# Optimization experiments

Hardware: AMD Instinct MI355X
Metric: run time of the kernel (lower is better)

## Reference

```python
import jax, jax.numpy as jnp
import numpy as np

BATCH = 1048576
D_IN = 4        # d_in=3 spatial dims + 1 time dim
HID = 64
N_HID_STACK = 4  # hidden residual blocks after the first hidden layer
D_OUT = 3
BN_EPS = 1e-5


def _bn(x, gamma, beta):
    # BatchNorm1d in training mode: biased batch statistics over the batch axis
    mu = jnp.mean(x, axis=0)
    var = jnp.var(x, axis=0)
    return gamma * (x - mu) * jax.lax.rsqrt(var + BN_EPS) + beta


def setup_inputs() -> dict:
    key = jax.random.key(0)
    ks = jax.random.split(key, 8)
    s_in = 1.0 / np.sqrt(D_IN)
    s_h = 1.0 / np.sqrt(HID)
    return {
        "x": jax.random.normal(ks[0], (BATCH, D_IN), dtype=jnp.float32),
        "bn0_gamma": jnp.ones((D_IN,), jnp.float32),
        "bn0_beta": jnp.zeros((D_IN,), jnp.float32),
        "W0": jax.random.normal(ks[1], (D_IN, HID), jnp.float32) * s_in,
        "b0": jnp.zeros((HID,), jnp.float32),
        "gamma0": jnp.ones((HID,), jnp.float32),
        "beta0": jnp.zeros((HID,), jnp.float32),
        "W_hid": jax.random.normal(ks[2], (N_HID_STACK, HID, HID), jnp.float32) * s_h,
        "b_hid": jnp.zeros((N_HID_STACK, HID), jnp.float32),
        "gamma_hid": jnp.ones((N_HID_STACK, HID), jnp.float32),
        "beta_hid": jnp.zeros((N_HID_STACK, HID), jnp.float32),
        "Wout": jax.random.normal(ks[3], (HID, D_OUT), jnp.float32) * s_h,
        "bout": jnp.zeros((D_OUT,), jnp.float32),
    }


def reference(x, bn0_gamma, bn0_beta, W0, b0, gamma0, beta0,
              W_hid, b_hid, gamma_hid, beta_hid, Wout, bout):
    # Net.forward (u-network, single patch, batch_normalization=True, tanh):
    #   x = bn0(x)
    #   y = bn(act(Linear0(x)))                 (first hidden layer, no skip)
    #   y = bn_i(act(Linear_i(y))) + y          (residual hidden layers)
    #   y = Linear_out(y)
    h = _bn(x, bn0_gamma, bn0_beta)
    y = _bn(jnp.tanh(h @ W0 + b0), gamma0, beta0)

    def step(y, layer):
        W, b, g, be = layer
        return _bn(jnp.tanh(y @ W + b), g, be) + y, None

    y, _ = jax.lax.scan(step, y, (W_hid, b_hid, gamma_hid, beta_hid))
    return y @ Wout + bout
```

## Files before the change

### kernel.cpp

```cpp
#include <hip/hip_runtime.h>
#include <stdint.h>


#define NROWS 1048576
#define EPS 1e-5f
#define INV_B 9.5367431640625e-07f
#define LOG2E2 2.885390081777927f
#define BIGGRID 16384

typedef __attribute__((ext_vector_type(8))) short bfrag;
typedef __attribute__((ext_vector_type(4))) float facc;
typedef __attribute__((ext_vector_type(4))) float f4v;

__device__ __forceinline__ float bf2f(short s) {
  union { unsigned u; float f; } v;
  v.u = ((unsigned)(unsigned short)s) << 16;
  return v.f;
}
__device__ __forceinline__ short f2bf(float f) {
  union { float f; unsigned u; } v;
  v.f = f;
  unsigned r = v.u + 0x7FFFu + ((v.u >> 16) & 1u);
  return (short)(r >> 16);
}
__device__ __forceinline__ float tanh_fast(float x) {
  float e = __builtin_amdgcn_exp2f(x * LOG2E2);
  return 1.f - 2.f * __builtin_amdgcn_rcpf(e + 1.f);
}

template <int W>
__global__ __launch_bounds__(256) void k_reduce(const float* __restrict__ P,
                                                float* __restrict__ S,
                                                int rows_per_blk) {
  __shared__ float red[256];
  const int tid = threadIdx.x;
  const int col = tid % W;
  const int grp = tid / W;
  const int G = 256 / W;
  size_t r0 = (size_t)blockIdx.x * rows_per_blk;
  float s = 0.f;
  for (int r = grp; r < rows_per_blk; r += G) s += P[(r0 + r) * W + col];
  red[tid] = s;
  __syncthreads();
  if (tid < W) {
    float t = 0.f;
#pragma unroll 4
    for (int g = 0; g < G; ++g) t += red[g * W + tid];
    atomicAdd(&S[tid], t);
  }
}


__global__ __launch_bounds__(256) void k_stats_x(const float* __restrict__ x,
                                                 float* __restrict__ P) {
  __shared__ float red[4][8];
  const int tid = threadIdx.x;
  const int wave = tid >> 6;
  size_t base = (size_t)blockIdx.x * 1024 + tid;
  float s[4] = {0.f, 0.f, 0.f, 0.f}, q[4] = {0.f, 0.f, 0.f, 0.f};
#pragma unroll
  for (int it = 0; it < 4; ++it) {
    f4v v = *(const f4v*)(x + (base + (size_t)it * 256) * 4);
#pragma unroll
    for (int k = 0; k < 4; ++k) { s[k] += v[k]; q[k] = fmaf(v[k], v[k], q[k]); }
  }
#pragma unroll
  for (int off = 32; off > 0; off >>= 1) {
#pragma unroll
    for (int k = 0; k < 4; ++k) {
      s[k] += __shfl_xor(s[k], off);
      q[k] += __shfl_xor(q[k], off);
    }
  }
  if ((tid & 63) == 0) {
#pragma unroll
    for (int k = 0; k < 4; ++k) { red[wave][k] = s[k]; red[wave][4 + k] = q[k]; }
  }
  __syncthreads();
  if (tid < 8)
    P[blockIdx.x * 8 + tid] =
        red[0][tid] + red[1][tid] + red[2][tid] + red[3][tid];
}

__global__ __launch_bounds__(256) void k_stats_z1(
    const float* __restrict__ x, const float* __restrict__ bn0g,
    const float* __restrict__ bn0b, const float* __restrict__ W0,
    const float* __restrict__ b0, const float* __restrict__ sx,
    float* __restrict__ P) {
  __shared__ float red[2][4][64];
  const int tid = threadIdx.x;
  const int lane = tid & 63;
  const int wave = tid >> 6;
  int gw = blockIdx.x * 4 + wave;
  float sc[4], sh[4];
#pragma unroll
  for (int k = 0; k < 4; ++k) {
    float mean = sx[k] * INV_B;
    float var = fmaf(-mean, mean, sx[4 + k] * INV_B);
    float rs = rsqrtf(var + EPS);
    sc[k] = bn0g[k] * rs;
    sh[k] = fmaf(-sc[k], mean, bn0b[k]);
  }
  float w[4];
#pragma unroll
  for (int k = 0; k < 4; ++k) w[k] = W0[k * 64 + lane];
  float bj = b0[lane];
  float s = 0.f, q = 0.f;
  size_t r0 = (size_t)gw * 256;
  for (int r = 0; r < 256; ++r) {
    f4v xv = *(const f4v*)(x + (r0 + r) * 4);
    float acc = bj;
#pragma unroll
    for (int k = 0; k < 4; ++k)
      acc = fmaf(fmaf(xv[k], sc[k], sh[k]), w[k], acc);
    float z = tanh_fast(acc);
    s += z;
    q = fmaf(z, z, q);
  }
  red[0][wave][lane] = s;
  red[1][wave][lane] = q;
  __syncthreads();
  if (tid < 128) {
    int which = tid >> 6, c = tid & 63;
    P[blockIdx.x * 128 + tid] = red[which][0][c] + red[which][1][c] +
                                red[which][2][c] + red[which][3][c];
  }
}

__global__ __launch_bounds__(256) void k_prep(const float* __restrict__ Wh,
                                              short* __restrict__ WT) {
  int idx = blockIdx.x * 256 + threadIdx.x;
  int l = idx >> 12, rem = idx & 4095, k = rem >> 6, c = rem & 63;
  WT[l * 4096 + c * 64 + k] = f2bf(Wh[l * 4096 + k * 64 + c]);
}


__global__ __launch_bounds__(128) void k_first(
    const float* __restrict__ x, const float* __restrict__ bn0g,
    const float* __restrict__ bn0b, const float* __restrict__ W0,
    const float* __restrict__ b0, const float* __restrict__ gamma0,
    const float* __restrict__ beta0, const float* __restrict__ sx,
    const float* __restrict__ s1, const short* __restrict__ WTb,
    const float* __restrict__ bb, float* __restrict__ P,
    short* __restrict__ Y) {
  __shared__ __align__(16) float lds_x[64 * 4];
  __shared__ __align__(16) short lds_y[64 * 72];
  __shared__ float lds_st[128];

  const int tid = threadIdx.x;
  const int lane = tid & 63;
  const int wave = tid >> 6;
  const int l15 = lane & 15;
  const int q = lane >> 4;
  const int wr = wave * 32;
  const size_t r0 = (size_t)blockIdx.x * 64;

  f4v xp;
  if (lane < 32) xp = *(const f4v*)(x + (r0 + wr + lane) * 4);

  lds_st[tid] = 0.f;
  float sc0[4], sh0[4];
#pragma unroll
  for (int k = 0; k < 4; ++k) {
    float mean = sx[k] * INV_B;
    float var = fmaf(-mean, mean, sx[4 + k] * INV_B);
    float rs = rsqrtf(var + EPS);
    sc0[k] = bn0g[k] * rs;
    sh0[k] = fmaf(-sc0[k], mean, bn0b[k]);
  }
  float w0c[4];
#pragma unroll
  for (int k = 0; k < 4; ++k) w0c[k] = W0[k * 64 + lane];
  float b0c = b0[lane];
  float mean1 = s1[lane] * INV_B;
  float var1 = fmaf(-mean1, mean1, s1[64 + lane] * INV_B);
  float A1c = gamma0[lane] * rsqrtf(var1 + EPS);
  float B1c = fmaf(-A1c, mean1, beta0[lane]);
  if (lane < 32) *(f4v*)&lds_x[(wr + lane) * 4] = xp;
  __syncthreads();

  for (int e = 0; e < 32; ++e) {
    int row = wr + e;
    float acc = b0c;
#pragma unroll
    for (int k = 0; k < 4; ++k)
      acc = fmaf(fmaf(lds_x[row * 4 + k], sc0[k], sh0[k]), w0c[k], acc);
    float z = tanh_fast(acc);
    lds_y[row * 72 + lane] = f2bf(fmaf(A1c, z, B1c));
  }

  bfrag af[2][2];
#pragma unroll
  for (int mt = 0; mt < 2; ++mt)
#pragma unroll
    for (int kt = 0; kt < 2; ++kt) {
      af[mt][kt] =
          *(const bfrag*)&lds_y[(wr + mt * 16 + l15) * 72 + kt * 32 + q * 8];
      *(bfrag*)(Y + (r0 + wr + mt * 16 + l15) * 64 + kt * 32 + q * 8) =
          af[mt][kt];
    }
  float bbv[4];
  bfrag bwb[4][2];
#pragma unroll
  for (int nt = 0; nt < 4; ++nt) {
    bbv[nt] = bb[nt * 16 + l15];
#pragma unroll
    for (int kt = 0; kt < 2; ++kt)
      bwb[nt][kt] =
          *(const bfrag*)(WTb + (nt * 16 + l15) * 64 + kt * 32 + q * 8);
  }
  facc acc2[2][4];
#pragma unroll
  for (int mt = 0; mt < 2; ++mt)
#pragma unroll
    for (int nt = 0; nt < 4; ++nt) {
      acc2[mt][nt][0] = bbv[nt]; acc2[mt][nt][1] = bbv[nt];
      acc2[mt][nt][2] = bbv[nt]; acc2[mt][nt][3] = bbv[nt];
    }
#pragma unroll
  for (int mt = 0; mt < 2; ++mt)
#pragma unroll
    for (int nt = 0; nt < 4; ++nt)
#pragma unroll
      for (int kt = 0; kt < 2; ++kt)
        acc2[mt][nt] = __builtin_amdgcn_mfma_f32_16x16x32_bf16(
            af[mt][kt], bwb[nt][kt], acc2[mt][nt], 0, 0, 0);
  float sAcc[4], qAcc[4];
#pragma unroll
  for (int nt = 0; nt < 4; ++nt) {
    sAcc[nt] = 0.f;
    qAcc[nt] = 0.f;
#pragma unroll
    for (int mt = 0; mt < 2; ++mt)
#pragma unroll
      for (int i = 0; i < 4; ++i) {
        float z = tanh_fast(acc2[mt][nt][i]);
        sAcc[nt] += z;
        qAcc[nt] = fmaf(z, z, qAcc[nt]);
      }
    float s = sAcc[nt], ss = qAcc[nt];
    s += __shfl_xor(s, 16); s += __shfl_xor(s, 32);
    ss += __shfl_xor(ss, 16); ss += __shfl_xor(ss, 32);
    if (q == 0) {
      atomicAdd(&lds_st[nt * 16 + l15], s);
      atomicAdd(&lds_st[64 + nt * 16 + l15], ss);
    }
  }
  __syncthreads();
  P[(size_t)blockIdx.x * 128 + tid] = lds_st[tid];
}

__global__ __launch_bounds__(128) void k_mid(
    short* __restrict__ Y, const short* __restrict__ WTa,
    const float* __restrict__ ba, const float* __restrict__ ga,
    const float* __restrict__ bea, const float* __restrict__ sa,
    const short* __restrict__ WTb, const float* __restrict__ bb,
    float* __restrict__ P) {
  __shared__ __align__(16) short lds_y[64 * 72];
  __shared__ float lds_st[128];

  const int tid = threadIdx.x;
  const int lane = tid & 63;
  const int wave = tid >> 6;
  const int l15 = lane & 15;
  const int q = lane >> 4;
  const int wr = wave * 32;
  const size_t r0 = (size_t)blockIdx.x * 64;
  const int srow = lane >> 3;
  const int sc8 = (lane & 7) * 8;

  bfrag ld[4];
  {
    const size_t g = (r0 + wr + srow) * 64 + sc8;
#pragma unroll
    for (int it = 0; it < 4; ++it)
      ld[it] = *(const bfrag*)(Y + g + (size_t)it * 8 * 64);
  }

  lds_st[tid] = 0.f;
  float Av[4], Bv[4], bav[4];
#pragma unroll
  for (int nt = 0; nt < 4; ++nt) {
    int c = nt * 16 + l15;
    float mean = sa[c] * INV_B;
    float var = fmaf(-mean, mean, sa[64 + c] * INV_B);
    float A = ga[c] * rsqrtf(var + EPS);
    Av[nt] = A;
    Bv[nt] = fmaf(-A, mean, bea[c]);
    bav[nt] = ba[c];
  }
  bfrag bwa[4][2];
#pragma unroll
  for (int nt = 0; nt < 4; ++nt)
#pragma unroll
    for (int kt = 0; kt < 2; ++kt)
      bwa[nt][kt] =
          *(const bfrag*)(WTa + (nt * 16 + l15) * 64 + kt * 32 + q * 8);

#pragma unroll
  for (int it = 0; it < 4; ++it)
    *(bfrag*)&lds_y[(wr + it * 8 + srow) * 72 + sc8] = ld[it];
  __syncthreads();

  bfrag af[2][2];
#pragma unroll
  for (int mt = 0; mt < 2; ++mt)
#pragma unroll
    for (int kt = 0; kt < 2; ++kt)
      af[mt][kt] =
          *(const bfrag*)&lds_y[(wr + mt * 16 + l15) * 72 + kt * 32 + q * 8];
  facc acc[2][4];
#pragma unroll
  for (int mt = 0; mt < 2; ++mt)
#pragma unroll
    for (int nt = 0; nt < 4; ++nt) {
      acc[mt][nt][0] = bav[nt]; acc[mt][nt][1] = bav[nt];
      acc[mt][nt][2] = bav[nt]; acc[mt][nt][3] = bav[nt];
    }
#pragma unroll
  for (int mt = 0; mt < 2; ++mt)
#pragma unroll
    for (int nt = 0; nt < 4; ++nt)
#pragma unroll
      for (int kt = 0; kt < 2; ++kt)
        acc[mt][nt] = __builtin_amdgcn_mfma_f32_16x16x32_bf16(
            af[mt][kt], bwa[nt][kt], acc[mt][nt], 0, 0, 0);

#pragma unroll
  for (int mt = 0; mt < 2; ++mt)
#pragma unroll
    for (int nt = 0; nt < 4; ++nt) {
      int c = nt * 16 + l15;
      float A = Av[nt], Bc = Bv[nt];
#pragma unroll
      for (int i = 0; i < 4; ++i) {
        int rl = wr + mt * 16 + q * 4 + i;
        float z = tanh_fast(acc[mt][nt][i]);
        float yo = bf2f(lds_y[rl * 72 + c]);
        lds_y[rl * 72 + c] = f2bf(fmaf(A, z, Bc) + yo);
      }
    }

#pragma unroll
  for (int mt = 0; mt < 2; ++mt)
#pragma unroll
    for (int kt = 0; kt < 2; ++kt) {
      af[mt][kt] =
          *(const bfrag*)&lds_y[(wr + mt * 16 + l15) * 72 + kt * 32 + q * 8];
      *(bfrag*)(Y + (r0 + wr + mt * 16 + l15) * 64 + kt * 32 + q * 8) =
          af[mt][kt];
    }
  float bbv[4];
  bfrag bwb[4][2];
#pragma unroll
  for (int nt = 0; nt < 4; ++nt) {
    bbv[nt] = bb[nt * 16 + l15];
#pragma unroll
    for (int kt = 0; kt < 2; ++kt)
      bwb[nt][kt] =
          *(const bfrag*)(WTb + (nt * 16 + l15) * 64 + kt * 32 + q * 8);
  }
#pragma unroll
  for (int mt = 0; mt < 2; ++mt)
#pragma unroll
    for (int nt = 0; nt < 4; ++nt) {
      acc[mt][nt][0] = bbv[nt]; acc[mt][nt][1] = bbv[nt];
      acc[mt][nt][2] = bbv[nt]; acc[mt][nt][3] = bbv[nt];
    }
#pragma unroll
  for (int mt = 0; mt < 2; ++mt)
#pragma unroll
    for (int nt = 0; nt < 4; ++nt)
#pragma unroll
      for (int kt = 0; kt < 2; ++kt)
        acc[mt][nt] = __builtin_amdgcn_mfma_f32_16x16x32_bf16(
            af[mt][kt], bwb[nt][kt], acc[mt][nt], 0, 0, 0);
#pragma unroll
  for (int nt = 0; nt < 4; ++nt) {
    float s = 0.f, ss = 0.f;
#pragma unroll
    for (int mt = 0; mt < 2; ++mt)
#pragma unroll
      for (int i = 0; i < 4; ++i) {
        float z = tanh_fast(acc[mt][nt][i]);
        s += z;
        ss = fmaf(z, z, ss);
      }
    s += __shfl_xor(s, 16); s += __shfl_xor(s, 32);
    ss += __shfl_xor(ss, 16); ss += __shfl_xor(ss, 32);
    if (q == 0) {
      atomicAdd(&lds_st[nt * 16 + l15], s);
      atomicAdd(&lds_st[64 + nt * 16 + l15], ss);
    }
  }
  __syncthreads();
  P[(size_t)blockIdx.x * 128 + tid] = lds_st[tid];
}

__global__ __launch_bounds__(128) void k_last(
    const short* __restrict__ Y, const short* __restrict__ WTa,
    const float* __restrict__ ba, const float* __restrict__ ga,
    const float* __restrict__ bea, const float* __restrict__ sa,
    const float* __restrict__ Wout, const float* __restrict__ bout,
    float* __restrict__ out) {
  __shared__ __align__(16) short lds_y[64 * 72];
  __shared__ float lds_wo[192];

  const int tid = threadIdx.x;
  const int lane = tid & 63;
  const int wave = tid >> 6;
  const int l15 = lane & 15;
  const int q = lane >> 4;
  const int wr = wave * 32;
  const size_t r0 = (size_t)blockIdx.x * 64;
  const int srow = lane >> 3;
  const int sc8 = (lane & 7) * 8;

  bfrag ld[4];
  {
    const size_t g = (r0 + wr + srow) * 64 + sc8;
#pragma unroll
    for (int it = 0; it < 4; ++it)
      ld[it] = *(const bfrag*)(Y + g + (size_t)it * 8 * 64);
  }

  for (int i = tid; i < 192; i += 128) lds_wo[i] = Wout[i];
  float Av[4], Bv[4], bav[4];
#pragma unroll
  for (int nt = 0; nt < 4; ++nt) {
    int c = nt * 16 + l15;
    float mean = sa[c] * INV_B;
    float var = fmaf(-mean, mean, sa[64 + c] * INV_B);
    float A = ga[c] * rsqrtf(var + EPS);
    Av[nt] = A;
    Bv[nt] = fmaf(-A, mean, bea[c]);
    bav[nt] = ba[c];
  }
  bfrag bwa[4][2];
#pragma unroll
  for (int nt = 0; nt < 4; ++nt)
#pragma unroll
    for (int kt = 0; kt < 2; ++kt)
      bwa[nt][kt] =
          *(const bfrag*)(WTa + (nt * 16 + l15) * 64 + kt * 32 + q * 8);
  float bo0 = bout[0], bo1 = bout[1], bo2 = bout[2];

#pragma unroll
  for (int it = 0; it < 4; ++it)
    *(bfrag*)&lds_y[(wr + it * 8 + srow) * 72 + sc8] = ld[it];
  __syncthreads();

  bfrag af[2][2];
#pragma unroll
  for (int mt = 0; mt < 2; ++mt)
#pragma unroll
    for (int kt = 0; kt < 2; ++kt)
      af[mt][kt] =
          *(const bfrag*)&lds_y[(wr + mt * 16 + l15) * 72 + kt * 32 + q * 8];
  facc acc[2][4];
#pragma unroll
  for (int mt = 0; mt < 2; ++mt)
#pragma unroll
    for (int nt = 0; nt < 4; ++nt) {
      acc[mt][nt][0] = bav[nt]; acc[mt][nt][1] = bav[nt];
      acc[mt][nt][2] = bav[nt]; acc[mt][nt][3] = bav[nt];
    }
#pragma unroll
  for (int mt = 0; mt < 2; ++mt)
#pragma unroll
    for (int nt = 0; nt < 4; ++nt)
#pragma unroll
      for (int kt = 0; kt < 2; ++kt)
        acc[mt][nt] = __builtin_amdgcn_mfma_f32_16x16x32_bf16(
            af[mt][kt], bwa[nt][kt], acc[mt][nt], 0, 0, 0);
#pragma unroll
  for (int mt = 0; mt < 2; ++mt)
#pragma unroll
    for (int nt = 0; nt < 4; ++nt) {
      int c = nt * 16 + l15;
      float A = Av[nt], Bc = Bv[nt];
#pragma unroll
      for (int i = 0; i < 4; ++i) {
        int rl = wr + mt * 16 + q * 4 + i;
        float z = tanh_fast(acc[mt][nt][i]);
        float yo = bf2f(lds_y[rl * 72 + c]);
        lds_y[rl * 72 + c] = f2bf(fmaf(A, z, Bc) + yo);
      }
    }

  {
    int row = wr + (lane >> 1);
    int cb = (lane & 1) * 32;
    float o0 = 0.f, o1 = 0.f, o2 = 0.f;
#pragma unroll
    for (int jc = 0; jc < 4; ++jc) {
      bfrag v = *(const bfrag*)&lds_y[row * 72 + cb + jc * 8];
#pragma unroll
      for (int j = 0; j < 8; ++j) {
        float f = bf2f(v[j]);
        int jj = cb + jc * 8 + j;
        o0 = fmaf(f, lds_wo[jj * 3 + 0], o0);
        o1 = fmaf(f, lds_wo[jj * 3 + 1], o1);
        o2 = fmaf(f, lds_wo[jj * 3 + 2], o2);
      }
    }
    o0 += __shfl_xor(o0, 1);
    o1 += __shfl_xor(o1, 1);
    o2 += __shfl_xor(o2, 1);
    if ((lane & 1) == 0) {
      size_t ro = (r0 + row) * 3;
      out[ro] = o0 + bo0;
      out[ro + 1] = o1 + bo1;
      out[ro + 2] = o2 + bo2;
    }
  }
}

extern "C" void kernel_launch(void* const* d_in, const int* in_sizes, int n_in,
                              void* d_out, int out_size, void* d_ws,
                              size_t ws_size, hipStream_t stream) {
  (void)in_sizes; (void)n_in; (void)out_size; (void)ws_size;
  const float* x = (const float*)d_in[0];
  const float* bn0g = (const float*)d_in[1];
  const float* bn0b = (const float*)d_in[2];
  const float* W0 = (const float*)d_in[3];
  const float* b0 = (const float*)d_in[4];
  const float* gamma0 = (const float*)d_in[5];
  const float* beta0 = (const float*)d_in[6];
  const float* Wh = (const float*)d_in[7];
  const float* bh = (const float*)d_in[8];
  const float* gh = (const float*)d_in[9];
  const float* beh = (const float*)d_in[10];
  const float* Wout = (const float*)d_in[11];
  const float* bout = (const float*)d_in[12];
  float* out = (float*)d_out;

  char* ws = (char*)d_ws;
  short* Y = (short*)ws;
  const size_t YB = (size_t)NROWS * 64 * 2;
  float* stats = (float*)(ws + YB);
  float* Sx = stats;
  float* S1 = stats + 8;
  float* S2 = stats + 136;
  float* S3 = stats + 264;
  float* S4 = stats + 392;
  float* S5 = stats + 520;
  short* WT = (short*)(ws + YB + 4096);
  float* P = (float*)(ws + YB + 4096 + 32768);

  hipMemsetAsync(stats, 0, 648 * sizeof(float), stream);
  k_prep<<<64, 256, 0, stream>>>(Wh, WT);
  k_stats_x<<<1024, 256, 0, stream>>>(x, P);
  k_reduce<8><<<8, 256, 0, stream>>>(P, Sx, 128);
  k_stats_z1<<<1024, 256, 0, stream>>>(x, bn0g, bn0b, W0, b0, Sx, P);
  k_reduce<128><<<8, 256, 0, stream>>>(P, S1, 128);
  k_first<<<BIGGRID, 128, 0, stream>>>(x, bn0g, bn0b, W0, b0, gamma0, beta0,
                                       Sx, S1, WT, bh, P, Y);
  k_reduce<128><<<128, 256, 0, stream>>>(P, S2, 128);
  k_mid<<<BIGGRID, 128, 0, stream>>>(Y, WT, bh, gh, beh, S2, WT + 4096,
                                     bh + 64, P);
  k_reduce<128><<<128, 256, 0, stream>>>(P, S3, 128);
  k_mid<<<BIGGRID, 128, 0, stream>>>(Y, WT + 4096, bh + 64, gh + 64, beh + 64,
                                     S3, WT + 2 * 4096, bh + 128, P);
  k_reduce<128><<<128, 256, 0, stream>>>(P, S4, 128);
  k_mid<<<BIGGRID, 128, 0, stream>>>(Y, WT + 2 * 4096, bh + 128, gh + 128,
                                     beh + 128, S4, WT + 3 * 4096, bh + 192, P);
  k_reduce<128><<<128, 256, 0, stream>>>(P, S5, 128);
  k_last<<<BIGGRID, 128, 0, stream>>>(Y, WT + 3 * 4096, bh + 192, gh + 192,
                                      beh + 192, S5, Wout, bout, out);
}
```

Before: 562.4 us.

## Use single-wave blocks processing two 32-row tiles with register prefetch

The main per-layer kernels now run with one 64-thread wave per block instead of two. Each wave handles both 32-row halves of its 64-row tile in sequence, prefetching the second half's activations into registers while the first half computes. This removes __syncthreads and the LDS atomics for the stats partials, which are now written directly from registers. It also loads Y fragments directly in MFMA layout rather than staging them through LDS. The cost is less in-block parallelism and a serial dependency between the two halves, while LDS per block is smaller, which may allow more blocks resident per CU.

```diff
diff --git a/kernel.cpp b/kernel.cpp
--- a/kernel.cpp
+++ b/kernel.cpp
@@ -135,7 +135,7 @@
 }
 
 
-__global__ __launch_bounds__(128) void k_first(
+__global__ __launch_bounds__(64) void k_first(
     const float* __restrict__ x, const float* __restrict__ bn0g,
     const float* __restrict__ bn0b, const float* __restrict__ W0,
     const float* __restrict__ b0, const float* __restrict__ gamma0,
@@ -143,22 +143,17 @@
     const float* __restrict__ s1, const short* __restrict__ WTb,
     const float* __restrict__ bb, float* __restrict__ P,
     short* __restrict__ Y) {
-  __shared__ __align__(16) float lds_x[64 * 4];
-  __shared__ __align__(16) short lds_y[64 * 72];
-  __shared__ float lds_st[128];
-
-  const int tid = threadIdx.x;
-  const int lane = tid & 63;
-  const int wave = tid >> 6;
+  __shared__ __align__(16) float lds_x[32 * 4];
+  __shared__ __align__(16) short ly[32 * 72];
+
+  const int lane = threadIdx.x & 63;
   const int l15 = lane & 15;
   const int q = lane >> 4;
-  const int wr = wave * 32;
   const size_t r0 = (size_t)blockIdx.x * 64;
 
   f4v xp;
-  if (lane < 32) xp = *(const f4v*)(x + (r0 + wr + lane) * 4);
-
-  lds_st[tid] = 0.f;
+  if (lane < 32) xp = *(const f4v*)(x + (r0 + lane) * 4);
+
   float sc0[4], sh0[4];
 #pragma unroll
   for (int k = 0; k < 4; ++k) {
@@ -176,29 +171,6 @@
   float var1 = fmaf(-mean1, mean1, s1[64 + lane] * INV_B);
   float A1c = gamma0[lane] * rsqrtf(var1 + EPS);
   float B1c = fmaf(-A1c, mean1, beta0[lane]);
-  if (lane < 32) *(f4v*)&lds_x[(wr + lane) * 4] = xp;
-  __syncthreads();
-
-  for (int e = 0; e < 32; ++e) {
-    int row = wr + e;
-    float acc = b0c;
-#pragma unroll
-    for (int k = 0; k < 4; ++k)
-      acc = fmaf(fmaf(lds_x[row * 4 + k], sc0[k], sh0[k]), w0c[k], acc);
-    float z = tanh_fast(acc);
-    lds_y[row * 72 + lane] = f2bf(fmaf(A1c, z, B1c));
-  }
-
-  bfrag af[2][2];
-#pragma unroll
-  for (int mt = 0; mt < 2; ++mt)
-#pragma unroll
-    for (int kt = 0; kt < 2; ++kt) {
-      af[mt][kt] =
-          *(const bfrag*)&lds_y[(wr + mt * 16 + l15) * 72 + kt * 32 + q * 8];
-      *(bfrag*)(Y + (r0 + wr + mt * 16 + l15) * 64 + kt * 32 + q * 8) =
-          af[mt][kt];
-    }
   float bbv[4];
   bfrag bwb[4][2];
 #pragma unroll
@@ -209,75 +181,95 @@
       bwb[nt][kt] =
           *(const bfrag*)(WTb + (nt * 16 + l15) * 64 + kt * 32 + q * 8);
   }
-  facc acc2[2][4];
-#pragma unroll
-  for (int mt = 0; mt < 2; ++mt)
-#pragma unroll
-    for (int nt = 0; nt < 4; ++nt) {
-      acc2[mt][nt][0] = bbv[nt]; acc2[mt][nt][1] = bbv[nt];
-      acc2[mt][nt][2] = bbv[nt]; acc2[mt][nt][3] = bbv[nt];
-    }
-#pragma unroll
-  for (int mt = 0; mt < 2; ++mt)
+
+  float sAcc[4] = {0.f, 0.f, 0.f, 0.f}, qAcc[4] = {0.f, 0.f, 0.f, 0.f};
+
+#pragma unroll
+  for (int t = 0; t < 2; ++t) {
+    const size_t rt = r0 + t * 32;
+    if (lane < 32) *(f4v*)&lds_x[lane * 4] = xp;
+    if (t == 0 && lane < 32) xp = *(const f4v*)(x + (r0 + 32 + lane) * 4);
+
+    for (int e = 0; e < 32; ++e) {
+      float acc = b0c;
+#pragma unroll
+      for (int k = 0; k < 4; ++k)
+        acc = fmaf(fmaf(lds_x[e * 4 + k], sc0[k], sh0[k]), w0c[k], acc);
+      float z = tanh_fast(acc);
+      ly[e * 72 + lane] = f2bf(fmaf(A1c, z, B1c));
+    }
+
+    bfrag af[2][2];
+#pragma unroll
+    for (int mt = 0; mt < 2; ++mt)
+#pragma unroll
+      for (int kt = 0; kt < 2; ++kt) {
+        af[mt][kt] =
+            *(const bfrag*)&ly[(mt * 16 + l15) * 72 + kt * 32 + q * 8];
+        *(bfrag*)(Y + (rt + mt * 16 + l15) * 64 + kt * 32 + q * 8) =
+            af[mt][kt];
+      }
+    facc acc2[2][4];
+#pragma unroll
+    for (int mt = 0; mt < 2; ++mt)
+#pragma unroll
+      for (int nt = 0; nt < 4; ++nt) {
+        acc2[mt][nt][0] = bbv[nt]; acc2[mt][nt][1] = bbv[nt];
+        acc2[mt][nt][2] = bbv[nt]; acc2[mt][nt][3] = bbv[nt];
+      }
+#pragma unroll
+    for (int mt = 0; mt < 2; ++mt)
+#pragma unroll
+      for (int nt = 0; nt < 4; ++nt)
+#pragma unroll
+        for (int kt = 0; kt < 2; ++kt)
+          acc2[mt][nt] = __builtin_amdgcn_mfma_f32_16x16x32_bf16(
+              af[mt][kt], bwb[nt][kt], acc2[mt][nt], 0, 0, 0);
 #pragma unroll
     for (int nt = 0; nt < 4; ++nt)
 #pragma unroll
-      for (int kt = 0; kt < 2; ++kt)
-        acc2[mt][nt] = __builtin_amdgcn_mfma_f32_16x16x32_bf16(
-            af[mt][kt], bwb[nt][kt], acc2[mt][nt], 0, 0, 0);
-  float sAcc[4], qAcc[4];
+      for (int mt = 0; mt < 2; ++mt)
+#pragma unroll
+        for (int i = 0; i < 4; ++i) {
+          float z = tanh_fast(acc2[mt][nt][i]);
+          sAcc[nt] += z;
+          qAcc[nt] = fmaf(z, z, qAcc[nt]);
+        }
+  }
+
 #pragma unroll
   for (int nt = 0; nt < 4; ++nt) {
-    sAcc[nt] = 0.f;
-    qAcc[nt] = 0.f;
-#pragma unroll
-    for (int mt = 0; mt < 2; ++mt)
-#pragma unroll
-      for (int i = 0; i < 4; ++i) {
-        float z = tanh_fast(acc2[mt][nt][i]);
-        sAcc[nt] += z;
-        qAcc[nt] = fmaf(z, z, qAcc[nt]);
-      }
     float s = sAcc[nt], ss = qAcc[nt];
     s += __shfl_xor(s, 16); s += __shfl_xor(s, 32);
     ss += __shfl_xor(ss, 16); ss += __shfl_xor(ss, 32);
     if (q == 0) {
-      atomicAdd(&lds_st[nt * 16 + l15], s);
-      atomicAdd(&lds_st[64 + nt * 16 + l15], ss);
-    }
-  }
-  __syncthreads();
-  P[(size_t)blockIdx.x * 128 + tid] = lds_st[tid];
-}
-
-__global__ __launch_bounds__(128) void k_mid(
+      P[(size_t)blockIdx.x * 128 + nt * 16 + l15] = s;
+      P[(size_t)blockIdx.x * 128 + 64 + nt * 16 + l15] = ss;
+    }
+  }
+}
+
+__global__ __launch_bounds__(64) void k_mid(
     short* __restrict__ Y, const short* __restrict__ WTa,
     const float* __restrict__ ba, const float* __restrict__ ga,
     const float* __restrict__ bea, const float* __restrict__ sa,
     const short* __restrict__ WTb, const float* __restrict__ bb,
     float* __restrict__ P) {
-  __shared__ __align__(16) short lds_y[64 * 72];
-  __shared__ float lds_st[128];
-
-  const int tid = threadIdx.x;
-  const int lane = tid & 63;
-  const int wave = tid >> 6;
+  __shared__ __align__(16) short ly[32 * 72];
+
+  const int lane = threadIdx.x & 63;
   const int l15 = lane & 15;
   const int q = lane >> 4;
-  const int wr = wave * 32;
   const size_t r0 = (size_t)blockIdx.x * 64;
-  const int srow = lane >> 3;
-  const int sc8 = (lane & 7) * 8;
-
-  bfrag ld[4];
-  {
-    const size_t g = (r0 + wr + srow) * 64 + sc8;
-#pragma unroll
-    for (int it = 0; it < 4; ++it)
-      ld[it] = *(const bfrag*)(Y + g + (size_t)it * 8 * 64);
-  }
-
-  lds_st[tid] = 0.f;
+
+  bfrag afn[2][2];
+#pragma unroll
+  for (int mt = 0; mt < 2; ++mt)
+#pragma unroll
+    for (int kt = 0; kt < 2; ++kt)
+      afn[mt][kt] =
+          *(const bfrag*)(Y + (r0 + mt * 16 + l15) * 64 + kt * 32 + q * 8);
+
   float Av[4], Bv[4], bav[4];
 #pragma unroll
   for (int nt = 0; nt < 4; ++nt) {
@@ -297,134 +289,142 @@
       bwa[nt][kt] =
           *(const bfrag*)(WTa + (nt * 16 + l15) * 64 + kt * 32 + q * 8);
 
-#pragma unroll
-  for (int it = 0; it < 4; ++it)
-    *(bfrag*)&lds_y[(wr + it * 8 + srow) * 72 + sc8] = ld[it];
-  __syncthreads();
-
-  bfrag af[2][2];
-#pragma unroll
-  for (int mt = 0; mt < 2; ++mt)
-#pragma unroll
-    for (int kt = 0; kt < 2; ++kt)
-      af[mt][kt] =
-          *(const bfrag*)&lds_y[(wr + mt * 16 + l15) * 72 + kt * 32 + q * 8];
-  facc acc[2][4];
-#pragma unroll
-  for (int mt = 0; mt < 2; ++mt)
+  float sAcc[4] = {0.f, 0.f, 0.f, 0.f}, qAcc[4] = {0.f, 0.f, 0.f, 0.f};
+
+#pragma unroll
+  for (int t = 0; t < 2; ++t) {
+    const size_t rt = r0 + t * 32;
+    bfrag af[2][2];
+#pragma unroll
+    for (int mt = 0; mt < 2; ++mt)
+#pragma unroll
+      for (int kt = 0; kt < 2; ++kt) {
+        af[mt][kt] = afn[mt][kt];
+        *(bfrag*)&ly[(mt * 16 + l15) * 72 + kt * 32 + q * 8] = af[mt][kt];
+      }
+    if (t == 0) {
+#pragma unroll
+      for (int mt = 0; mt < 2; ++mt)
+#pragma unroll
+        for (int kt = 0; kt < 2; ++kt)
+          afn[mt][kt] = *(const bfrag*)(Y + (r0 + 32 + mt * 16 + l15) * 64 +
+                                        kt * 32 + q * 8);
+    }
+
+    facc acc[2][4];
+#pragma unroll
+    for (int mt = 0; mt < 2; ++mt)
+#pragma unroll
+      for (int nt = 0; nt < 4; ++nt) {
+        acc[mt][nt][0] = bav[nt]; acc[mt][nt][1] = bav[nt];
+        acc[mt][nt][2] = bav[nt]; acc[mt][nt][3] = bav[nt];
+      }
+#pragma unroll
+    for (int mt = 0; mt < 2; ++mt)
+#pragma unroll
+      for (int nt = 0; nt < 4; ++nt)
+#pragma unroll
+        for (int kt = 0; kt < 2; ++kt)
+          acc[mt][nt] = __builtin_amdgcn_mfma_f32_16x16x32_bf16(
+              af[mt][kt], bwa[nt][kt], acc[mt][nt], 0, 0, 0);
+
+#pragma unroll
+    for (int mt = 0; mt < 2; ++mt)
+#pragma unroll
+      for (int nt = 0; nt < 4; ++nt) {
+        int c = nt * 16 + l15;
+        float A = Av[nt], Bc = Bv[nt];
+#pragma unroll
+        for (int i = 0; i < 4; ++i) {
+          int rl = mt * 16 + q * 4 + i;
+          float z = tanh_fast(acc[mt][nt][i]);
+          float yo = bf2f(ly[rl * 72 + c]);
+          ly[rl * 72 + c] = f2bf(fmaf(A, z, Bc) + yo);
+        }
+      }
+
+    bfrag af2[2][2];
+#pragma unroll
+    for (int mt = 0; mt < 2; ++mt)
+#pragma unroll
+      for (int kt = 0; kt < 2; ++kt) {
+        af2[mt][kt] =
+            *(const bfrag*)&ly[(mt * 16 + l15) * 72 + kt * 32 + q * 8];
+        *(bfrag*)(Y + (rt + mt * 16 + l15) * 64 + kt * 32 + q * 8) =
+            af2[mt][kt];
+      }
+    float bbv[4];
+    bfrag bwb[4][2];
 #pragma unroll
     for (int nt = 0; nt < 4; ++nt) {
-      acc[mt][nt][0] = bav[nt]; acc[mt][nt][1] = bav[nt];
-      acc[mt][nt][2] = bav[nt]; acc[mt][nt][3] = bav[nt];
-    }
-#pragma unroll
-  for (int mt = 0; mt < 2; ++mt)
+      bbv[nt] = bb[nt * 16 + l15];
+#pragma unroll
+      for (int kt = 0; kt < 2; ++kt)
+        bwb[nt][kt] =
+            *(const bfrag*)(WTb + (nt * 16 + l15) * 64 + kt * 32 + q * 8);
+    }
+#pragma unroll
+    for (int mt = 0; mt < 2; ++mt)
+#pragma unroll
+      for (int nt = 0; nt < 4; ++nt) {
+        acc[mt][nt][0] = bbv[nt]; acc[mt][nt][1] = bbv[nt];
+        acc[mt][nt][2] = bbv[nt]; acc[mt][nt][3] = bbv[nt];
+      }
+#pragma unroll
+    for (int mt = 0; mt < 2; ++mt)
+#pragma unroll
+      for (int nt = 0; nt < 4; ++nt)
+#pragma unroll
+        for (int kt = 0; kt < 2; ++kt)
+          acc[mt][nt] = __builtin_amdgcn_mfma_f32_16x16x32_bf16(
+              af2[mt][kt], bwb[nt][kt], acc[mt][nt], 0, 0, 0);
 #pragma unroll
     for (int nt = 0; nt < 4; ++nt)
 #pragma unroll
-      for (int kt = 0; kt < 2; ++kt)
-        acc[mt][nt] = __builtin_amdgcn_mfma_f32_16x16x32_bf16(
-            af[mt][kt], bwa[nt][kt], acc[mt][nt], 0, 0, 0);
-
-#pragma unroll
-  for (int mt = 0; mt < 2; ++mt)
-#pragma unroll
-    for (int nt = 0; nt < 4; ++nt) {
-      int c = nt * 16 + l15;
-      float A = Av[nt], Bc = Bv[nt];
-#pragma unroll
-      for (int i = 0; i < 4; ++i) {
-        int rl = wr + mt * 16 + q * 4 + i;
-        float z = tanh_fast(acc[mt][nt][i]);
-        float yo = bf2f(lds_y[rl * 72 + c]);
-        lds_y[rl * 72 + c] = f2bf(fmaf(A, z, Bc) + yo);
-      }
-    }
-
-#pragma unroll
-  for (int mt = 0; mt < 2; ++mt)
-#pragma unroll
-    for (int kt = 0; kt < 2; ++kt) {
-      af[mt][kt] =
-          *(const bfrag*)&lds_y[(wr + mt * 16 + l15) * 72 + kt * 32 + q * 8];
-      *(bfrag*)(Y + (r0 + wr + mt * 16 + l15) * 64 + kt * 32 + q * 8) =
-          af[mt][kt];
-    }
-  float bbv[4];
-  bfrag bwb[4][2];
+      for (int mt = 0; mt < 2; ++mt)
+#pragma unroll
+        for (int i = 0; i < 4; ++i) {
+          float z = tanh_fast(acc[mt][nt][i]);
+          sAcc[nt] += z;
+          qAcc[nt] = fmaf(z, z, qAcc[nt]);
+        }
+  }
+
 #pragma unroll
   for (int nt = 0; nt < 4; ++nt) {
-    bbv[nt] = bb[nt * 16 + l15];
-#pragma unroll
-    for (int kt = 0; kt < 2; ++kt)
-      bwb[nt][kt] =
-          *(const bfrag*)(WTb + (nt * 16 + l15) * 64 + kt * 32 + q * 8);
-  }
-#pragma unroll
-  for (int mt = 0; mt < 2; ++mt)
-#pragma unroll
-    for (int nt = 0; nt < 4; ++nt) {
-      acc[mt][nt][0] = bbv[nt]; acc[mt][nt][1] = bbv[nt];
-      acc[mt][nt][2] = bbv[nt]; acc[mt][nt][3] = bbv[nt];
-    }
-#pragma unroll
-  for (int mt = 0; mt < 2; ++mt)
-#pragma unroll
-    for (int nt = 0; nt < 4; ++nt)
-#pragma unroll
-      for (int kt = 0; kt < 2; ++kt)
-        acc[mt][nt] = __builtin_amdgcn_mfma_f32_16x16x32_bf16(
-            af[mt][kt], bwb[nt][kt], acc[mt][nt], 0, 0, 0);
-#pragma unroll
-  for (int nt = 0; nt < 4; ++nt) {
-    float s = 0.f, ss = 0.f;
-#pragma unroll
-    for (int mt = 0; mt < 2; ++mt)
-#pragma unroll
-      for (int i = 0; i < 4; ++i) {
-        float z = tanh_fast(acc[mt][nt][i]);
-        s += z;
-        ss = fmaf(z, z, ss);
-      }
+    float s = sAcc[nt], ss = qAcc[nt];
     s += __shfl_xor(s, 16); s += __shfl_xor(s, 32);
     ss += __shfl_xor(ss, 16); ss += __shfl_xor(ss, 32);
     if (q == 0) {
-      atomicAdd(&lds_st[nt * 16 + l15], s);
-      atomicAdd(&lds_st[64 + nt * 16 + l15], ss);
-    }
-  }
-  __syncthreads();
-  P[(size_t)blockIdx.x * 128 + tid] = lds_st[tid];
-}
-
-__global__ __launch_bounds__(128) void k_last(
+      P[(size_t)blockIdx.x * 128 + nt * 16 + l15] = s;
+      P[(size_t)blockIdx.x * 128 + 64 + nt * 16 + l15] = ss;
+    }
+  }
+}
+
+__global__ __launch_bounds__(64) void k_last(
     const short* __restrict__ Y, const short* __restrict__ WTa,
     const float* __restrict__ ba, const float* __restrict__ ga,
     const float* __restrict__ bea, const float* __restrict__ sa,
     const float* __restrict__ Wout, const float* __restrict__ bout,
     float* __restrict__ out) {
-  __shared__ __align__(16) short lds_y[64 * 72];
+  __shared__ __align__(16) short ly[32 * 72];
   __shared__ float lds_wo[192];
 
-  const int tid = threadIdx.x;
-  const int lane = tid & 63;
-  const int wave = tid >> 6;
+  const int lane = threadIdx.x & 63;
   const int l15 = lane & 15;
   const int q = lane >> 4;
-  const int wr = wave * 32;
   const size_t r0 = (size_t)blockIdx.x * 64;
-  const int srow = lane >> 3;
-  const int sc8 = (lane & 7) * 8;
-
-  bfrag ld[4];
-  {
-    const size_t g = (r0 + wr + srow) * 64 + sc8;
-#pragma unroll
-    for (int it = 0; it < 4; ++it)
-      ld[it] = *(const bfrag*)(Y + g + (size_t)it * 8 * 64);
-  }
-
-  for (int i = tid; i < 192; i += 128) lds_wo[i] = Wout[i];
+
+  bfrag afn[2][2];
+#pragma unroll
+  for (int mt = 0; mt < 2; ++mt)
+#pragma unroll
+    for (int kt = 0; kt < 2; ++kt)
+      afn[mt][kt] =
+          *(const bfrag*)(Y + (r0 + mt * 16 + l15) * 64 + kt * 32 + q * 8);
+
+  for (int i = lane; i < 192; i += 64) lds_wo[i] = Wout[i];
   float Av[4], Bv[4], bav[4];
 #pragma unroll
   for (int nt = 0; nt < 4; ++nt) {
@@ -446,72 +446,81 @@
   float bo0 = bout[0], bo1 = bout[1], bo2 = bout[2];
 
 #pragma unroll
-  for (int it = 0; it < 4; ++it)
-    *(bfrag*)&lds_y[(wr + it * 8 + srow) * 72 + sc8] = ld[it];
-  __syncthreads();
-
-  bfrag af[2][2];
-#pragma unroll
-  for (int mt = 0; mt < 2; ++mt)
-#pragma unroll
-    for (int kt = 0; kt < 2; ++kt)
-      af[mt][kt] =
-          *(const bfrag*)&lds_y[(wr + mt * 16 + l15) * 72 + kt * 32 + q * 8];
-  facc acc[2][4];
-#pragma unroll
-  for (int mt = 0; mt < 2; ++mt)
-#pragma unroll
-    for (int nt = 0; nt < 4; ++nt) {
-      acc[mt][nt][0] = bav[nt]; acc[mt][nt][1] = bav[nt];
-      acc[mt][nt][2] = bav[nt]; acc[mt][nt][3] = bav[nt];
-    }
-#pragma unroll
-  for (int mt = 0; mt < 2; ++mt)
-#pragma unroll
-    for (int nt = 0; nt < 4; ++nt)
-#pragma unroll
-      for (int kt = 0; kt < 2; ++kt)
-        acc[mt][nt] = __builtin_amdgcn_mfma_f32_16x16x32_bf16(
-            af[mt][kt], bwa[nt][kt], acc[mt][nt], 0, 0, 0);
-#pragma unroll
-  for (int mt = 0; mt < 2; ++mt)
-#pragma unroll
-    for (int nt = 0; nt < 4; ++nt) {
-      int c = nt * 16 + l15;
-      float A = Av[nt], Bc = Bv[nt];
-#pragma unroll
-      for (int i = 0; i < 4; ++i) {
-        int rl = wr + mt * 16 + q * 4 + i;
-        float z = tanh_fast(acc[mt][nt][i]);
-        float yo = bf2f(lds_y[rl * 72 + c]);
-        lds_y[rl * 72 + c] = f2bf(fmaf(A, z, Bc) + yo);
-      }
-    }
-
-  {
-    int row = wr + (lane >> 1);
-    int cb = (lane & 1) * 32;
-    float o0 = 0.f, o1 = 0.f, o2 = 0.f;
-#pragma unroll
-    for (int jc = 0; jc < 4; ++jc) {
-      bfrag v = *(const bfrag*)&lds_y[row * 72 + cb + jc * 8];
-#pragma unroll
-      for (int j = 0; j < 8; ++j) {
-        float f = bf2f(v[j]);
-        int jj = cb + jc * 8 + j;
-        o0 = fmaf(f, lds_wo[jj * 3 + 0], o0);
-        o1 = fmaf(f, lds_wo[jj * 3 + 1], o1);
-        o2 = fmaf(f, lds_wo[jj * 3 + 2], o2);
-      }
-    }
-    o0 += __shfl_xor(o0, 1);
-    o1 += __shfl_xor(o1, 1);
-    o2 += __shfl_xor(o2, 1);
-    if ((lane & 1) == 0) {
-      size_t ro = (r0 + row) * 3;
-      out[ro] = o0 + bo0;
-      out[ro + 1] = o1 + bo1;
-      out[ro + 2] = o2 + bo2;
+  for (int t = 0; t < 2; ++t) {
+    const size_t rt = r0 + t * 32;
+    bfrag af[2][2];
+#pragma unroll
+    for (int mt = 0; mt < 2; ++mt)
+#pragma unroll
+      for (int kt = 0; kt < 2; ++kt) {
+        af[mt][kt] = afn[mt][kt];
+        *(bfrag*)&ly[(mt * 16 + l15) * 72 + kt * 32 + q * 8] = af[mt][kt];
+      }
+    if (t == 0) {
+#pragma unroll
+      for (int mt = 0; mt < 2; ++mt)
+#pragma unroll
+        for (int kt = 0; kt < 2; ++kt)
+          afn[mt][kt] = *(const bfrag*)(Y + (r0 + 32 + mt * 16 + l15) * 64 +
+                                        kt * 32 + q * 8);
+    }
+
+    facc acc[2][4];
+#pragma unroll
+    for (int mt = 0; mt < 2; ++mt)
+#pragma unroll
+      for (int nt = 0; nt < 4; ++nt) {
+        acc[mt][nt][0] = bav[nt]; acc[mt][nt][1] = bav[nt];
+        acc[mt][nt][2] = bav[nt]; acc[mt][nt][3] = bav[nt];
+      }
+#pragma unroll
+    for (int mt = 0; mt < 2; ++mt)
+#pragma unroll
+      for (int nt = 0; nt < 4; ++nt)
+#pragma unroll
+        for (int kt = 0; kt < 2; ++kt)
+          acc[mt][nt] = __builtin_amdgcn_mfma_f32_16x16x32_bf16(
+              af[mt][kt], bwa[nt][kt], acc[mt][nt], 0, 0, 0);
+#pragma unroll
+    for (int mt = 0; mt < 2; ++mt)
+#pragma unroll
+      for (int nt = 0; nt < 4; ++nt) {
+        int c = nt * 16 + l15;
+        float A = Av[nt], Bc = Bv[nt];
+#pragma unroll
+        for (int i = 0; i < 4; ++i) {
+          int rl = mt * 16 + q * 4 + i;
+          float z = tanh_fast(acc[mt][nt][i]);
+          float yo = bf2f(ly[rl * 72 + c]);
+          ly[rl * 72 + c] = f2bf(fmaf(A, z, Bc) + yo);
+        }
+      }
+
+    {
+      int row = lane >> 1;
+      int cb = (lane & 1) * 32;
+      float o0 = 0.f, o1 = 0.f, o2 = 0.f;
+#pragma unroll
+      for (int jc = 0; jc < 4; ++jc) {
+        bfrag v = *(const bfrag*)&ly[row * 72 + cb + jc * 8];
+#pragma unroll
+        for (int j = 0; j < 8; ++j) {
+          float f = bf2f(v[j]);
+          int jj = cb + jc * 8 + j;
+          o0 = fmaf(f, lds_wo[jj * 3 + 0], o0);
+          o1 = fmaf(f, lds_wo[jj * 3 + 1], o1);
+          o2 = fmaf(f, lds_wo[jj * 3 + 2], o2);
+        }
+      }
+      o0 += __shfl_xor(o0, 1);
+      o1 += __shfl_xor(o1, 1);
+      o2 += __shfl_xor(o2, 1);
+      if ((lane & 1) == 0) {
+        size_t ro = (rt + row) * 3;
+        out[ro] = o0 + bo0;
+        out[ro + 1] = o1 + bo1;
+        out[ro + 2] = o2 + bo2;
+      }
     }
   }
 }
@@ -554,18 +563,18 @@
   k_reduce<8><<<8, 256, 0, stream>>>(P, Sx, 128);
   k_stats_z1<<<1024, 256, 0, stream>>>(x, bn0g, bn0b, W0, b0, Sx, P);
   k_reduce<128><<<8, 256, 0, stream>>>(P, S1, 128);
-  k_first<<<BIGGRID, 128, 0, stream>>>(x, bn0g, bn0b, W0, b0, gamma0, beta0,
-                                       Sx, S1, WT, bh, P, Y);
+  k_first<<<BIGGRID, 64, 0, stream>>>(x, bn0g, bn0b, W0, b0, gamma0, beta0,
+                                      Sx, S1, WT, bh, P, Y);
   k_reduce<128><<<128, 256, 0, stream>>>(P, S2, 128);
-  k_mid<<<BIGGRID, 128, 0, stream>>>(Y, WT, bh, gh, beh, S2, WT + 4096,
-                                     bh + 64, P);
+  k_mid<<<BIGGRID, 64, 0, stream>>>(Y, WT, bh, gh, beh, S2, WT + 4096,
+                                    bh + 64, P);
   k_reduce<128><<<128, 256, 0, stream>>>(P, S3, 128);
-  k_mid<<<BIGGRID, 128, 0, stream>>>(Y, WT + 4096, bh + 64, gh + 64, beh + 64,
-                                     S3, WT + 2 * 4096, bh + 128, P);
+  k_mid<<<BIGGRID, 64, 0, stream>>>(Y, WT + 4096, bh + 64, gh + 64, beh + 64,
+                                    S3, WT + 2 * 4096, bh + 128, P);
   k_reduce<128><<<128, 256, 0, stream>>>(P, S4, 128);
-  k_mid<<<BIGGRID, 128, 0, stream>>>(Y, WT + 2 * 4096, bh + 128, gh + 128,
-                                     beh + 128, S4, WT + 3 * 4096, bh + 192, P);
+  k_mid<<<BIGGRID, 64, 0, stream>>>(Y, WT + 2 * 4096, bh + 128, gh + 128,
+                                    beh + 128, S4, WT + 3 * 4096, bh + 192, P);
   k_reduce<128><<<128, 256, 0, stream>>>(P, S5, 128);
-  k_last<<<BIGGRID, 128, 0, stream>>>(Y, WT + 3 * 4096, bh + 192, gh + 192,
-                                      beh + 192, S5, Wout, bout, out);
-}
+  k_last<<<BIGGRID, 64, 0, stream>>>(Y, WT + 3 * 4096, bh + 192, gh + 192,
+                                     beh + 192, S5, Wout, bout, out);
+}
```

Measured after the change: 569.6 us. About the same (+1.3%).
